# Performance work log

Hardware: AMD Instinct MI355X
Metric: run time of the kernel (lower is better)

## Reference

```python
import jax, jax.numpy as jnp
import numpy as np

N_NODES = 50000
N_EDGES = 800000
IN_DIM = 128
HID = 256
HEADS = 4
OUT_DIM = 128
NEG_SLOPE = 0.2


def gat_conv(x, src, dst, W, a_src, a_dst, b, heads, out_ch):
    """PyG-style GATConv: per-edge attention + segment softmax over dst."""
    N = x.shape[0]
    h = (x @ W).reshape(N, heads, out_ch)              # [N,H,C]
    alph_s = jnp.einsum('nhc,hc->nh', h, a_src)        # [N,H]
    alph_d = jnp.einsum('nhc,hc->nh', h, a_dst)        # [N,H]
    e = jax.nn.leaky_relu(alph_s[src] + alph_d[dst], NEG_SLOPE)  # [E,H]
    m = jax.lax.stop_gradient(jax.ops.segment_max(e, dst, num_segments=N))
    ex = jnp.exp(e - m[dst])
    s = jax.ops.segment_sum(ex, dst, num_segments=N)
    alpha = ex / (s[dst] + 1e-16)                      # [E,H]
    out = jax.ops.segment_sum(h[src] * alpha[:, :, None], dst, num_segments=N)
    return out.reshape(N, heads * out_ch) + b


def setup_inputs() -> dict:
    key = jax.random.key(0)
    ks = jax.random.split(key, 12)
    x = jax.random.normal(ks[0], (N_NODES, IN_DIM), dtype=jnp.float32)
    edge_index = jax.random.randint(ks[1], (2, N_EDGES), 0, N_NODES, dtype=jnp.int64)
    c1 = HID // HEADS  # 64
    sc1 = 1.0 / np.sqrt(IN_DIM)
    sc2 = 1.0 / np.sqrt(HID)
    W1 = jax.random.normal(ks[2], (IN_DIM, HID), dtype=jnp.float32) * sc1
    a1_src = jax.random.normal(ks[3], (HEADS, c1), dtype=jnp.float32) * sc1
    a1_dst = jax.random.normal(ks[4], (HEADS, c1), dtype=jnp.float32) * sc1
    b1 = jnp.zeros((HID,), dtype=jnp.float32)
    W2 = jax.random.normal(ks[5], (HID, OUT_DIM), dtype=jnp.float32) * sc2
    a2_src = jax.random.normal(ks[6], (1, OUT_DIM), dtype=jnp.float32) * sc2
    a2_dst = jax.random.normal(ks[7], (1, OUT_DIM), dtype=jnp.float32) * sc2
    b2 = jnp.zeros((OUT_DIM,), dtype=jnp.float32)
    return {"x": x, "edge_index": edge_index, "W1": W1, "a1_src": a1_src,
            "a1_dst": a1_dst, "b1": b1, "W2": W2, "a2_src": a2_src,
            "a2_dst": a2_dst, "b2": b2}


def reference(x, edge_index, W1, a1_src, a1_dst, b1, W2, a2_src, a2_dst, b2):
    N = x.shape[0]
    loops = jnp.arange(N, dtype=edge_index.dtype)
    # PyG default add_self_loops=True
    src = jnp.concatenate([edge_index[0], loops])
    dst = jnp.concatenate([edge_index[1], loops])
    h = jax.nn.relu(gat_conv(x, src, dst, W1, a1_src, a1_dst, b1, HEADS, HID // HEADS))
    # dropout is identity in eval mode
    return gat_conv(h, src, dst, W2, a2_src, a2_dst, b2, 1, OUT_DIM)
```

## Files before the change

### kernel.cpp

```cpp
#include <hip/hip_runtime.h>
#include <math.h>

#define NEG_SLOPE 0.2f
#define SLOTS 64
#define ECAP 63

typedef __attribute__((ext_vector_type(8))) short bf16x8;
typedef __attribute__((ext_vector_type(4))) float f32x4;
typedef __attribute__((ext_vector_type(2))) float f32x2;

__device__ __forceinline__ float lrelu(float t) {
    return t > 0.f ? t : NEG_SLOPE * t;
}
__device__ __forceinline__ unsigned short f2bf(float f) {
    unsigned u = __float_as_uint(f);
    unsigned r = (u + 0x7fff + ((u >> 16) & 1)) >> 16;
    return (unsigned short)r;
}
__device__ __forceinline__ f32x2 unpack2(unsigned v) {
    f32x2 r;
    r.x = __uint_as_float(v << 16);
    r.y = __uint_as_float(v & 0xffff0000u);
    return r;
}

__global__ void prep0(const float* __restrict__ W1, const float* __restrict__ a1s,
                      const float* __restrict__ a1d, float* __restrict__ vsd1,
                      const float* __restrict__ W2, const float* __restrict__ a2s,
                      const float* __restrict__ a2d, float* __restrict__ vsd2) {
    int i = blockIdx.x * 256 + threadIdx.x;
    if (i < 512) {
        int k = i >> 2, h = i & 3;
        float s = 0.f, d = 0.f;
        for (int c = 0; c < 64; c++) {
            float wv = W1[k * 256 + h * 64 + c];
            s += wv * a1s[h * 64 + c];
            d += wv * a1d[h * 64 + c];
        }
        vsd1[h * 128 + k] = s;
        vsd1[(4 + h) * 128 + k] = d;
    } else if (i < 768) {
        int j = i - 512;
        float s = 0.f, d = 0.f;
        for (int c = 0; c < 128; c++) {
            float wv = W2[j * 128 + c];
            s += wv * a2s[c];
            d += wv * a2d[c];
        }
        vsd2[j] = s;
        vsd2[256 + j] = d;
    }
}

__global__ void mega(const int* __restrict__ src, const int* __restrict__ dst,
                     int* __restrict__ cursor, unsigned short* __restrict__ eSrc,
                     const float* __restrict__ x, uint4* __restrict__ xb4,
                     const float* __restrict__ W1, unsigned short* __restrict__ W1t,
                     const float* __restrict__ W2, unsigned short* __restrict__ W2t,
                     const float* __restrict__ vsd1,
                     float* __restrict__ as1, float* __restrict__ ad1,
                     int E, int N, int bS, int bC, int bW1, int bW2) {
    __shared__ float vs[1024];
    const int b = blockIdx.x, t = threadIdx.x;
    if (b < bS) {
        int i4 = (b * 256 + t) * 4;
        if (i4 + 3 < E) {
            const int4 s4 = *(const int4*)(src + i4);
            const int4 d4 = *(const int4*)(dst + i4);
            int p0 = atomicAdd(&cursor[d4.x], 1);
            int p1 = atomicAdd(&cursor[d4.y], 1);
            int p2 = atomicAdd(&cursor[d4.z], 1);
            int p3 = atomicAdd(&cursor[d4.w], 1);
            if (p0 < ECAP) eSrc[(d4.x << 6) + p0] = (unsigned short)s4.x;
            if (p1 < ECAP) eSrc[(d4.y << 6) + p1] = (unsigned short)s4.y;
            if (p2 < ECAP) eSrc[(d4.z << 6) + p2] = (unsigned short)s4.z;
            if (p3 < ECAP) eSrc[(d4.w << 6) + p3] = (unsigned short)s4.w;
        } else {
            for (int k = i4; k < E && k < i4 + 4; k++) {
                int d = dst[k];
                int pos = atomicAdd(&cursor[d], 1);
                if (pos < ECAP) eSrc[(d << 6) + pos] = (unsigned short)src[k];
            }
        }
    } else if (b < bC) {
        int i = (b - bS) * 256 + t;
        if (i < N * 16) {
            const float4* x4 = (const float4*)x;
            float4 v0 = x4[2 * i], v1 = x4[2 * i + 1];
            uint4 o;
            o.x = (unsigned)f2bf(v0.x) | ((unsigned)f2bf(v0.y) << 16);
            o.y = (unsigned)f2bf(v0.z) | ((unsigned)f2bf(v0.w) << 16);
            o.z = (unsigned)f2bf(v1.x) | ((unsigned)f2bf(v1.y) << 16);
            o.w = (unsigned)f2bf(v1.z) | ((unsigned)f2bf(v1.w) << 16);
            xb4[i] = o;
        }
    } else if (b < bW1) {
        int i = (b - bC) * 256 + t;
        int n = i >> 7, k = i & 127;
        W1t[i] = f2bf(W1[k * 256 + n]);
    } else if (b < bW2) {
        int i = (b - bW1) * 256 + t;
        int n = i >> 8, k = i & 255;
        W2t[i] = f2bf(W2[k * 128 + n]);
    } else {
        for (int i = t; i < 1024; i += 256) vs[i] = vsd1[i];
        __syncthreads();
        int wave = t >> 6, lane = t & 63;
        int n = (b - bW2) * 4 + wave;
        if (n >= N) return;
        float acc[8];
#pragma unroll
        for (int j = 0; j < 8; j++) acc[j] = 0.f;
#pragma unroll
        for (int i = 0; i < 2; i++) {
            float xv = x[(size_t)n * 128 + i * 64 + lane];
#pragma unroll
            for (int j = 0; j < 8; j++) acc[j] += xv * vs[j * 128 + i * 64 + lane];
        }
#pragma unroll
        for (int off = 32; off > 0; off >>= 1) {
#pragma unroll
            for (int j = 0; j < 8; j++) acc[j] += __shfl_down(acc[j], off, 64);
        }
        if (lane == 0) {
#pragma unroll
            for (int h = 0; h < 4; h++) {
                as1[n * 4 + h] = acc[h];
                ad1[n * 4 + h] = acc[4 + h];
            }
        }
    }
}

template <int K, int N>
__global__ __launch_bounds__(256) void gemm_mfma(const unsigned short* __restrict__ A,
                                                 const unsigned short* __restrict__ Bt,
                                                 unsigned short* __restrict__ Cb, int M) {
    constexpr int LDT = 72;
    __shared__ __align__(16) short As[128 * LDT];
    __shared__ __align__(16) short Bs[64 * LDT];
    const int t = threadIdx.x;
    const int wave = t >> 6, lane = t & 63;
    const int row0 = blockIdx.x * 128;
    const int n0 = blockIdx.y * 64;

    f32x4 acc[2][4];
#pragma unroll
    for (int mt = 0; mt < 2; mt++)
#pragma unroll
        for (int nt = 0; nt < 4; nt++) acc[mt][nt] = (f32x4){0.f, 0.f, 0.f, 0.f};

    const int r = t >> 3, c8 = (t & 7) * 8;
    for (int kc = 0; kc < K; kc += 64) {
        const unsigned short* srcA = A + (size_t)row0 * K + kc;
#pragma unroll
        for (int p = 0; p < 4; p++) {
            int rr = r + p * 32;
            *(bf16x8*)&As[rr * LDT + c8] = *(const bf16x8*)&srcA[(size_t)rr * K + c8];
        }
        const unsigned short* srcB = Bt + (size_t)n0 * K + kc;
#pragma unroll
        for (int p = 0; p < 2; p++) {
            int rr = r + p * 32;
            *(bf16x8*)&Bs[rr * LDT + c8] = *(const bf16x8*)&srcB[(size_t)rr * K + c8];
        }
        __syncthreads();

        const int mbase = wave * 32 + (lane & 15);
        const int quad = lane >> 4;
#pragma unroll
        for (int ks = 0; ks < 2; ks++) {
            int ko = ks * 32 + quad * 8;
            bf16x8 a0 = *(const bf16x8*)&As[mbase * LDT + ko];
            bf16x8 a1 = *(const bf16x8*)&As[(mbase + 16) * LDT + ko];
#pragma unroll
            for (int nt = 0; nt < 4; nt++) {
                bf16x8 b = *(const bf16x8*)&Bs[((lane & 15) + nt * 16) * LDT + ko];
                acc[0][nt] = __builtin_amdgcn_mfma_f32_16x16x32_bf16(a0, b, acc[0][nt], 0, 0, 0);
                acc[1][nt] = __builtin_amdgcn_mfma_f32_16x16x32_bf16(a1, b, acc[1][nt], 0, 0, 0);
            }
        }
        __syncthreads();
    }

    const int colb = n0 + (lane & 15);
    const int rquad = (lane >> 4) * 4;
#pragma unroll
    for (int mt = 0; mt < 2; mt++) {
        int rb = row0 + wave * 32 + mt * 16 + rquad;
#pragma unroll
        for (int nt = 0; nt < 4; nt++) {
#pragma unroll
            for (int rr2 = 0; rr2 < 4; rr2++) {
                int row = rb + rr2;
                if (row < M) Cb[(size_t)row * N + colb + nt * 16] = f2bf(acc[mt][nt][rr2]);
            }
        }
    }
}

__global__ __launch_bounds__(256) void gemm1_head(
    const unsigned short* __restrict__ agg, const unsigned short* __restrict__ W1t,
    const float* __restrict__ b1, const float* __restrict__ vsd2,
    unsigned short* __restrict__ out1b, float* __restrict__ as2, float* __restrict__ ad2,
    int M, int Mpad) {
    constexpr int K = 128, LDT = 72;
    __shared__ __align__(16) short As[128 * LDT];
    __shared__ __align__(16) short Bs[64 * LDT];
    const int t = threadIdx.x;
    const int wave = t >> 6, lane = t & 63;
    const int row0 = blockIdx.x * 128;
    const int h = blockIdx.y;
    const unsigned short* A = agg + (size_t)h * Mpad * K;
    const unsigned short* Bt = W1t + (size_t)h * 64 * K;

    f32x4 acc[2][4];
#pragma unroll
    for (int mt = 0; mt < 2; mt++)
#pragma unroll
        for (int nt = 0; nt < 4; nt++) acc[mt][nt] = (f32x4){0.f, 0.f, 0.f, 0.f};

    const int r = t >> 3, c8 = (t & 7) * 8;
    for (int kc = 0; kc < K; kc += 64) {
        const unsigned short* srcA = A + (size_t)row0 * K + kc;
#pragma unroll
        for (int p = 0; p < 4; p++) {
            int rr = r + p * 32;
            *(bf16x8*)&As[rr * LDT + c8] = *(const bf16x8*)&srcA[(size_t)rr * K + c8];
        }
        const unsigned short* srcB = Bt + kc;
#pragma unroll
        for (int p = 0; p < 2; p++) {
            int rr = r + p * 32;
            *(bf16x8*)&Bs[rr * LDT + c8] = *(const bf16x8*)&srcB[(size_t)rr * K + c8];
        }
        __syncthreads();

        const int mbase = wave * 32 + (lane & 15);
        const int quad = lane >> 4;
#pragma unroll
        for (int ks = 0; ks < 2; ks++) {
            int ko = ks * 32 + quad * 8;
            bf16x8 a0 = *(const bf16x8*)&As[mbase * LDT + ko];
            bf16x8 a1 = *(const bf16x8*)&As[(mbase + 16) * LDT + ko];
#pragma unroll
            for (int nt = 0; nt < 4; nt++) {
                bf16x8 b = *(const bf16x8*)&Bs[((lane & 15) + nt * 16) * LDT + ko];
                acc[0][nt] = __builtin_amdgcn_mfma_f32_16x16x32_bf16(a0, b, acc[0][nt], 0, 0, 0);
                acc[1][nt] = __builtin_amdgcn_mfma_f32_16x16x32_bf16(a1, b, acc[1][nt], 0, 0, 0);
            }
        }
        __syncthreads();
    }

    const int col16 = lane & 15;
    const int grp = lane >> 4;
#pragma unroll
    for (int mt = 0; mt < 2; mt++) {
        int rb = row0 + wave * 32 + mt * 16 + grp * 4;
#pragma unroll
        for (int rr = 0; rr < 4; rr++) {
            int row = rb + rr;
            float ps = 0.f, pd = 0.f;
#pragma unroll
            for (int nt = 0; nt < 4; nt++) {
                int cg = h * 64 + col16 + nt * 16;
                float rres = acc[mt][nt][rr] + b1[cg];
                rres = fmaxf(rres, 0.f);
                if (row < M) out1b[(size_t)row * 256 + cg] = f2bf(rres);
                ps += rres * vsd2[cg];
                pd += rres * vsd2[256 + cg];
            }
#pragma unroll
            for (int mask = 1; mask < 16; mask <<= 1) {
                ps += __shfl_xor(ps, mask, 64);
                pd += __shfl_xor(pd, mask, 64);
            }
            if (col16 == 0 && row < M) {
                atomicAdd(&as2[row], ps);
                atomicAdd(&ad2[row], pd);
            }
        }
    }
}

__global__ __launch_bounds__(256) void fused_gather1(
    const int* __restrict__ cursor, const unsigned short* __restrict__ eSrc,
    const unsigned short* __restrict__ Xb,
    const float* __restrict__ as_, const float* __restrict__ ad_,
    unsigned short* __restrict__ agg, int N, int Mpad) {
    const int wv = threadIdx.x >> 6, lane = threadIdx.x & 63;
    const int half = lane >> 5, hl = lane & 31;
    const int d = blockIdx.x * 8 + wv * 2 + half;

    __shared__ float4 alS[4][2][64];
    __shared__ int offS[4][2][64];

    const bool vn = d < N;
    int deg = 0;
    if (vn) { deg = cursor[d]; if (deg > ECAP) deg = ECAP; }
    float4 adv = make_float4(0.f, 0.f, 0.f, 0.f);
    if (vn) adv = ((const float4*)ad_)[d];

    const int beg = d << 6;
    const int j0 = hl, j1 = hl + 32;
    const bool a0 = vn && (j0 <= deg), a1 = vn && (j1 <= deg);
    int s0 = vn ? d : 0, s1 = vn ? d : 0;
    if (vn && j0 < deg) s0 = eSrc[beg + j0];
    if (vn && j1 < deg) s1 = eSrc[beg + j1];
    float4 q0 = make_float4(0.f, 0.f, 0.f, 0.f), q1 = q0;
    if (a0) q0 = ((const float4*)as_)[s0];
    if (a1) q1 = ((const float4*)as_)[s1];

    float qa0[4] = {q0.x, q0.y, q0.z, q0.w};
    float qa1[4] = {q1.x, q1.y, q1.z, q1.w};
    float ad4[4] = {adv.x, adv.y, adv.z, adv.w};
    float e0[4], e1[4], m[4];
#pragma unroll
    for (int h = 0; h < 4; h++) {
        e0[h] = a0 ? lrelu(qa0[h] + ad4[h]) : -1e30f;
        e1[h] = a1 ? lrelu(qa1[h] + ad4[h]) : -1e30f;
        m[h] = fmaxf(e0[h], e1[h]);
    }
#pragma unroll
    for (int off = 1; off < 32; off <<= 1)
#pragma unroll
        for (int h = 0; h < 4; h++) m[h] = fmaxf(m[h], __shfl_xor(m[h], off, 64));
    float x0[4], x1[4], sum[4];
#pragma unroll
    for (int h = 0; h < 4; h++) {
        x0[h] = a0 ? __expf(e0[h] - m[h]) : 0.f;
        x1[h] = a1 ? __expf(e1[h] - m[h]) : 0.f;
        sum[h] = x0[h] + x1[h];
    }
#pragma unroll
    for (int off = 1; off < 32; off <<= 1)
#pragma unroll
        for (int h = 0; h < 4; h++) sum[h] += __shfl_xor(sum[h], off, 64);
    float ri[4];
#pragma unroll
    for (int h = 0; h < 4; h++) ri[h] = 1.f / (sum[h] + 1e-16f);

    alS[wv][half][j0] = make_float4(x0[0] * ri[0], x0[1] * ri[1], x0[2] * ri[2], x0[3] * ri[3]);
    alS[wv][half][j1] = make_float4(x1[0] * ri[0], x1[1] * ri[1], x1[2] * ri[2], x1[3] * ri[3]);
    offS[wv][half][j0] = s0 << 8;
    offS[wv][half][j1] = s1 << 8;

    int rows = vn ? deg + 1 : 0;
    { int o = __shfl_xor(rows, 32, 64); rows = rows > o ? rows : o; }

    const char* Xc = (const char*)Xb;
    const int myoff = hl * 8;
    f32x2 acc[4][2];
#pragma unroll
    for (int h = 0; h < 4; h++) { acc[h][0] = (f32x2){0.f, 0.f}; acc[h][1] = (f32x2){0.f, 0.f}; }

    int j = 0;
    for (; j + 3 < rows; j += 4) {
        int o0 = offS[wv][half][j], o1 = offS[wv][half][j + 1];
        int o2 = offS[wv][half][j + 2], o3 = offS[wv][half][j + 3];
        uint2 v0 = *(const uint2*)(Xc + o0 + myoff);
        uint2 v1 = *(const uint2*)(Xc + o1 + myoff);
        uint2 v2 = *(const uint2*)(Xc + o2 + myoff);
        uint2 v3 = *(const uint2*)(Xc + o3 + myoff);
        float4 al0 = alS[wv][half][j];
        float4 al1 = alS[wv][half][j + 1];
        float4 al2 = alS[wv][half][j + 2];
        float4 al3 = alS[wv][half][j + 3];
        {
            f32x2 lo = unpack2(v0.x), hi = unpack2(v0.y);
            acc[0][0] += al0.x * lo; acc[0][1] += al0.x * hi;
            acc[1][0] += al0.y * lo; acc[1][1] += al0.y * hi;
            acc[2][0] += al0.z * lo; acc[2][1] += al0.z * hi;
            acc[3][0] += al0.w * lo; acc[3][1] += al0.w * hi;
        }
        {
            f32x2 lo = unpack2(v1.x), hi = unpack2(v1.y);
            acc[0][0] += al1.x * lo; acc[0][1] += al1.x * hi;
            acc[1][0] += al1.y * lo; acc[1][1] += al1.y * hi;
            acc[2][0] += al1.z * lo; acc[2][1] += al1.z * hi;
            acc[3][0] += al1.w * lo; acc[3][1] += al1.w * hi;
        }
        {
            f32x2 lo = unpack2(v2.x), hi = unpack2(v2.y);
            acc[0][0] += al2.x * lo; acc[0][1] += al2.x * hi;
            acc[1][0] += al2.y * lo; acc[1][1] += al2.y * hi;
            acc[2][0] += al2.z * lo; acc[2][1] += al2.z * hi;
            acc[3][0] += al2.w * lo; acc[3][1] += al2.w * hi;
        }
        {
            f32x2 lo = unpack2(v3.x), hi = unpack2(v3.y);
            acc[0][0] += al3.x * lo; acc[0][1] += al3.x * hi;
            acc[1][0] += al3.y * lo; acc[1][1] += al3.y * hi;
            acc[2][0] += al3.z * lo; acc[2][1] += al3.z * hi;
            acc[3][0] += al3.w * lo; acc[3][1] += al3.w * hi;
        }
    }
    for (; j < rows; j++) {
        int o0 = offS[wv][half][j];
        uint2 v0 = *(const uint2*)(Xc + o0 + myoff);
        float4 al0 = alS[wv][half][j];
        f32x2 lo = unpack2(v0.x), hi = unpack2(v0.y);
        acc[0][0] += al0.x * lo; acc[0][1] += al0.x * hi;
        acc[1][0] += al0.y * lo; acc[1][1] += al0.y * hi;
        acc[2][0] += al0.z * lo; acc[2][1] += al0.z * hi;
        acc[3][0] += al0.w * lo; acc[3][1] += al0.w * hi;
    }

    if (vn) {
#pragma unroll
        for (int h = 0; h < 4; h++) {
            uint2 pack;
            pack.x = (unsigned)f2bf(acc[h][0].x) | ((unsigned)f2bf(acc[h][0].y) << 16);
            pack.y = (unsigned)f2bf(acc[h][1].x) | ((unsigned)f2bf(acc[h][1].y) << 16);
            ((uint2*)(agg + ((size_t)h * Mpad + d) * 128))[hl] = pack;
        }
    }
}

__global__ __launch_bounds__(256) void fused_gather2(
    const int* __restrict__ cursor, const unsigned short* __restrict__ eSrc,
    const unsigned short* __restrict__ Hb,
    const float* __restrict__ as_, const float* __restrict__ ad_,
    const float* __restrict__ b2, float* __restrict__ out, int N) {
    const int wv = threadIdx.x >> 6, lane = threadIdx.x & 63;
    const int half = lane >> 5, hl = lane & 31;
    const int d = blockIdx.x * 8 + wv * 2 + half;

    __shared__ float alS[4][2][64];
    __shared__ int offS[4][2][64];

    const bool vn = d < N;
    int deg = 0;
    if (vn) { deg = cursor[d]; if (deg > ECAP) deg = ECAP; }
    const float adv = vn ? ad_[d] : 0.f;

    const int beg = d << 6;
    const int j0 = hl, j1 = hl + 32;
    const bool a0 = vn && (j0 <= deg), a1 = vn && (j1 <= deg);
    int s0 = vn ? d : 0, s1 = vn ? d : 0;
    if (vn && j0 < deg) s0 = eSrc[beg + j0];
    if (vn && j1 < deg) s1 = eSrc[beg + j1];
    float e0 = a0 ? lrelu(as_[s0] + adv) : -1e30f;
    float e1 = a1 ? lrelu(as_[s1] + adv) : -1e30f;
    float m = fmaxf(e0, e1);
#pragma unroll
    for (int off = 1; off < 32; off <<= 1) m = fmaxf(m, __shfl_xor(m, off, 64));
    float x0 = a0 ? __expf(e0 - m) : 0.f;
    float x1 = a1 ? __expf(e1 - m) : 0.f;
    float sum = x0 + x1;
#pragma unroll
    for (int off = 1; off < 32; off <<= 1) sum += __shfl_xor(sum, off, 64);
    float ri = 1.f / (sum + 1e-16f);

    alS[wv][half][j0] = x0 * ri;
    alS[wv][half][j1] = x1 * ri;
    offS[wv][half][j0] = s0 << 8;
    offS[wv][half][j1] = s1 << 8;

    int rows = vn ? deg + 1 : 0;
    { int o = __shfl_xor(rows, 32, 64); rows = rows > o ? rows : o; }

    const char* Hc = (const char*)Hb;
    const int myoff = hl * 8;
    f32x2 acc0 = (f32x2){0.f, 0.f}, acc1 = (f32x2){0.f, 0.f};

    int j = 0;
    for (; j + 3 < rows; j += 4) {
        int o0 = offS[wv][half][j], o1 = offS[wv][half][j + 1];
        int o2 = offS[wv][half][j + 2], o3 = offS[wv][half][j + 3];
        uint2 v0 = *(const uint2*)(Hc + o0 + myoff);
        uint2 v1 = *(const uint2*)(Hc + o1 + myoff);
        uint2 v2 = *(const uint2*)(Hc + o2 + myoff);
        uint2 v3 = *(const uint2*)(Hc + o3 + myoff);
        float b0 = alS[wv][half][j], b1v = alS[wv][half][j + 1];
        float b2v = alS[wv][half][j + 2], b3 = alS[wv][half][j + 3];
        acc0 += b0 * unpack2(v0.x); acc1 += b0 * unpack2(v0.y);
        acc0 += b1v * unpack2(v1.x); acc1 += b1v * unpack2(v1.y);
        acc0 += b2v * unpack2(v2.x); acc1 += b2v * unpack2(v2.y);
        acc0 += b3 * unpack2(v3.x); acc1 += b3 * unpack2(v3.y);
    }
    for (; j < rows; j++) {
        int o0 = offS[wv][half][j];
        uint2 v0 = *(const uint2*)(Hc + o0 + myoff);
        float b0 = alS[wv][half][j];
        acc0 += b0 * unpack2(v0.x); acc1 += b0 * unpack2(v0.y);
    }

    if (vn) {
        float4 bb = ((const float4*)b2)[hl];
        float4 o;
        o.x = acc0.x + bb.x;
        o.y = acc0.y + bb.y;
        o.z = acc1.x + bb.z;
        o.w = acc1.y + bb.w;
        ((float4*)(out + (size_t)d * 128))[hl] = o;
    }
}

extern "C" void kernel_launch(void* const* d_in, const int* in_sizes, int n_in,
                              void* d_out, int out_size, void* d_ws, size_t ws_size,
                              hipStream_t stream) {
    const float* x   = (const float*)d_in[0];
    const int*   ei  = (const int*)d_in[1];
    const float* W1  = (const float*)d_in[2];
    const float* a1s = (const float*)d_in[3];
    const float* a1d = (const float*)d_in[4];
    const float* b1  = (const float*)d_in[5];
    const float* W2  = (const float*)d_in[6];
    const float* a2s = (const float*)d_in[7];
    const float* a2d = (const float*)d_in[8];
    const float* b2  = (const float*)d_in[9];

    const int N = in_sizes[0] / 128;
    const int E = in_sizes[1] / 2;
    const int* srcIdx = ei;
    const int* dstIdx = ei + E;
    float* out = (float*)d_out;

    const int MT = (N + 127) / 128;
    const int M_pad = MT * 128;

    char* w = (char*)d_ws;
    unsigned short* x_bf  = (unsigned short*)w; w += (size_t)N * 128 * 2;
    unsigned short* agg   = (unsigned short*)w; w += (size_t)4 * M_pad * 128 * 2;
    unsigned short* out1b = (unsigned short*)w; w += (size_t)M_pad * 256 * 2;
    unsigned short* h2b   = (unsigned short*)w; w += (size_t)N * 128 * 2;
    unsigned short* W1t   = (unsigned short*)w; w += (size_t)128 * 256 * 2;
    unsigned short* W2t   = (unsigned short*)w; w += (size_t)256 * 128 * 2;
    float* vsd1 = (float*)w; w += (size_t)128 * 8 * 4;
    float* vsd2 = (float*)w; w += (size_t)256 * 2 * 4;
    float* as1  = (float*)w; w += (size_t)N * 4 * 4;
    float* ad1  = (float*)w; w += (size_t)N * 4 * 4;
    float* as2  = (float*)w; w += (size_t)N * 4;
    float* ad2  = (float*)w; w += (size_t)N * 4;
    int* cursor = (int*)w;  w += (size_t)N * 4;
    unsigned short* eSrc = (unsigned short*)w; w += (size_t)N * SLOTS * 2;

    hipMemsetAsync(cursor, 0, (size_t)N * 4, stream);
    hipMemsetAsync(as2, 0, (size_t)N * 4, stream);
    hipMemsetAsync(ad2, 0, (size_t)N * 4, stream);

    prep0<<<3, 256, 0, stream>>>(W1, a1s, a1d, vsd1, W2, a2s, a2d, vsd2);

    {
        const int bS  = (E + 1023) / 1024;
        const int nC  = (N * 16 + 255) / 256;
        const int bC  = bS + nC;
        const int bW1 = bC + 128;
        const int bW2 = bW1 + 128;
        const int nG  = (N + 3) / 4;
        mega<<<bW2 + nG, 256, 0, stream>>>(srcIdx, dstIdx, cursor, eSrc,
                                           x, (uint4*)x_bf, W1, W1t, W2, W2t,
                                           vsd1, as1, ad1, E, N, bS, bC, bW1, bW2);
    }

    fused_gather1<<<(N + 7) / 8, 256, 0, stream>>>(cursor, eSrc, x_bf, as1, ad1, agg, N, M_pad);
    gemm1_head<<<dim3(MT, 4), 256, 0, stream>>>(agg, W1t, b1, vsd2, out1b, as2, ad2, N, M_pad);

    gemm_mfma<256, 128><<<dim3(MT, 2), 256, 0, stream>>>(out1b, W2t, h2b, N);
    fused_gather2<<<(N + 7) / 8, 256, 0, stream>>>(cursor, eSrc, h2b, as2, ad2, b2, out, N);
}
```

Before: 294.1 us.

## Build CSR via two-pass bucketed binning with LDS atomics

Replaces per-edge global atomics on the per-node cursor with a two-level scheme. Each block counts edges per 128-node bucket in shared memory, reserves ranges with one global atomic per bucket, and scatters packed (local dst, src) words into bucket bins. A new build_csr kernel then places edges into per-node slots in LDS and writes them out coalesced. This targets scattered global atomic contention and uncoalesced 2-byte writes, at the cost of an extra kernel launch, bin traffic through the reused agg buffer, and a fixed per-bucket capacity that could drop edges on skewed graphs.

```diff
diff --git a/kernel.cpp b/kernel.cpp
--- a/kernel.cpp
+++ b/kernel.cpp
@@ -4,6 +4,8 @@
 #define NEG_SLOPE 0.2f
 #define SLOTS 64
 #define ECAP 63
+#define NBMAX 391
+#define BCAP 2432
 
 typedef __attribute__((ext_vector_type(8))) short bf16x8;
 typedef __attribute__((ext_vector_type(4))) float f32x4;
@@ -52,38 +54,72 @@
     }
 }
 
+#define EMIT(dd, ss)                                                     \
+    {                                                                    \
+        int bk_ = (dd) >> 7;                                             \
+        int pos_ = atomicAdd(&cntS[bk_], 1);                             \
+        if (pos_ < BCAP)                                                 \
+            bin[(size_t)bk_ * BCAP + pos_] =                             \
+                ((unsigned)((dd) & 127) << 16) | (unsigned)(ss);         \
+    }
+
 __global__ void mega(const int* __restrict__ src, const int* __restrict__ dst,
-                     int* __restrict__ cursor, unsigned short* __restrict__ eSrc,
+                     int* __restrict__ gcur, unsigned* __restrict__ bin,
                      const float* __restrict__ x, uint4* __restrict__ xb4,
                      const float* __restrict__ W1, unsigned short* __restrict__ W1t,
                      const float* __restrict__ W2, unsigned short* __restrict__ W2t,
                      const float* __restrict__ vsd1,
                      float* __restrict__ as1, float* __restrict__ ad1,
-                     int E, int N, int bS, int bC, int bW1, int bW2) {
+                     int E, int N, int nb, int bP1, int bC, int bW1, int bW2) {
     __shared__ float vs[1024];
+    __shared__ int cntS[NBMAX];
     const int b = blockIdx.x, t = threadIdx.x;
-    if (b < bS) {
-        int i4 = (b * 256 + t) * 4;
-        if (i4 + 3 < E) {
-            const int4 s4 = *(const int4*)(src + i4);
-            const int4 d4 = *(const int4*)(dst + i4);
-            int p0 = atomicAdd(&cursor[d4.x], 1);
-            int p1 = atomicAdd(&cursor[d4.y], 1);
-            int p2 = atomicAdd(&cursor[d4.z], 1);
-            int p3 = atomicAdd(&cursor[d4.w], 1);
-            if (p0 < ECAP) eSrc[(d4.x << 6) + p0] = (unsigned short)s4.x;
-            if (p1 < ECAP) eSrc[(d4.y << 6) + p1] = (unsigned short)s4.y;
-            if (p2 < ECAP) eSrc[(d4.z << 6) + p2] = (unsigned short)s4.z;
-            if (p3 < ECAP) eSrc[(d4.w << 6) + p3] = (unsigned short)s4.w;
-        } else {
-            for (int k = i4; k < E && k < i4 + 4; k++) {
-                int d = dst[k];
-                int pos = atomicAdd(&cursor[d], 1);
-                if (pos < ECAP) eSrc[(d << 6) + pos] = (unsigned short)src[k];
-            }
-        }
+    if (b < bP1) {
+        for (int i = t; i < nb; i += 256) cntS[i] = 0;
+        __syncthreads();
+        const int4* s4p = (const int4*)src;
+        const int4* d4p = (const int4*)dst;
+        const int E4 = E >> 2;
+        int4 sv[4], dv[4];
+        bool act[4];
+#pragma unroll
+        for (int i = 0; i < 4; i++) {
+            int idx = b * 1024 + i * 256 + t;
+            act[i] = idx < E4;
+            sv[i] = act[i] ? s4p[idx] : (int4){0, 0, 0, 0};
+            dv[i] = act[i] ? d4p[idx] : (int4){0, 0, 0, 0};
+        }
+        int exd = -1, exs = 0;
+        if (b == 0 && (E4 << 2) + t < E) {
+            exd = dst[(E4 << 2) + t];
+            exs = src[(E4 << 2) + t];
+        }
+#pragma unroll
+        for (int i = 0; i < 4; i++)
+            if (act[i]) {
+                atomicAdd(&cntS[dv[i].x >> 7], 1);
+                atomicAdd(&cntS[dv[i].y >> 7], 1);
+                atomicAdd(&cntS[dv[i].z >> 7], 1);
+                atomicAdd(&cntS[dv[i].w >> 7], 1);
+            }
+        if (exd >= 0) atomicAdd(&cntS[exd >> 7], 1);
+        __syncthreads();
+        for (int i = t; i < nb; i += 256) {
+            int c = cntS[i];
+            cntS[i] = c ? atomicAdd(&gcur[i], c) : 0;
+        }
+        __syncthreads();
+#pragma unroll
+        for (int i = 0; i < 4; i++)
+            if (act[i]) {
+                EMIT(dv[i].x, sv[i].x);
+                EMIT(dv[i].y, sv[i].y);
+                EMIT(dv[i].z, sv[i].z);
+                EMIT(dv[i].w, sv[i].w);
+            }
+        if (exd >= 0) EMIT(exd, exs);
     } else if (b < bC) {
-        int i = (b - bS) * 256 + t;
+        int i = (b - bP1) * 256 + t;
         if (i < N * 16) {
             const float4* x4 = (const float4*)x;
             float4 v0 = x4[2 * i], v1 = x4[2 * i + 1];
@@ -130,6 +166,32 @@
             }
         }
     }
+}
+
+__global__ __launch_bounds__(256) void build_csr(const int* __restrict__ gcur,
+                                                 const unsigned* __restrict__ bin,
+                                                 unsigned short* __restrict__ eSrc,
+                                                 int* __restrict__ cursor) {
+    __shared__ unsigned short slotS[128 * 64];
+    __shared__ int lc[128];
+    const int b = blockIdx.x, t = threadIdx.x;
+    if (t < 128) lc[t] = 0;
+    __syncthreads();
+    int cnt = gcur[b];
+    if (cnt > BCAP) cnt = BCAP;
+    const unsigned* bb = bin + (size_t)b * BCAP;
+    for (int i = t; i < cnt; i += 256) {
+        unsigned e = bb[i];
+        int dl = e >> 16;
+        int p = atomicAdd(&lc[dl], 1);
+        if (p < ECAP) slotS[(dl << 6) + p] = (unsigned short)(e & 0xffff);
+    }
+    __syncthreads();
+    const uint4* sp = (const uint4*)slotS;
+    uint4* dp = (uint4*)(eSrc + ((size_t)b << 13));
+#pragma unroll
+    for (int i = 0; i < 4; i++) dp[t + i * 256] = sp[t + i * 256];
+    if (t < 128) cursor[(b << 7) + t] = lc[t];
 }
 
 template <int K, int N>
@@ -520,6 +582,7 @@
 
     const int MT = (N + 127) / 128;
     const int M_pad = MT * 128;
+    const int nb = (N + 127) >> 7;
 
     char* w = (char*)d_ws;
     unsigned short* x_bf  = (unsigned short*)w; w += (size_t)N * 128 * 2;
@@ -534,26 +597,30 @@
     float* ad1  = (float*)w; w += (size_t)N * 4 * 4;
     float* as2  = (float*)w; w += (size_t)N * 4;
     float* ad2  = (float*)w; w += (size_t)N * 4;
-    int* cursor = (int*)w;  w += (size_t)N * 4;
-    unsigned short* eSrc = (unsigned short*)w; w += (size_t)N * SLOTS * 2;
-
-    hipMemsetAsync(cursor, 0, (size_t)N * 4, stream);
+    int* cursor = (int*)w;  w += (size_t)M_pad * 4;
+    unsigned short* eSrc = (unsigned short*)w; w += (size_t)M_pad * SLOTS * 2;
+    int* gcur = (int*)w; w += (size_t)nb * 4;
+    unsigned* bin = (unsigned*)agg;
+
+    hipMemsetAsync(gcur, 0, (size_t)nb * 4, stream);
     hipMemsetAsync(as2, 0, (size_t)N * 4, stream);
     hipMemsetAsync(ad2, 0, (size_t)N * 4, stream);
 
     prep0<<<3, 256, 0, stream>>>(W1, a1s, a1d, vsd1, W2, a2s, a2d, vsd2);
 
     {
-        const int bS  = (E + 1023) / 1024;
+        const int bP1 = (E / 4 + 1023) / 1024;
         const int nC  = (N * 16 + 255) / 256;
-        const int bC  = bS + nC;
+        const int bC  = bP1 + nC;
         const int bW1 = bC + 128;
         const int bW2 = bW1 + 128;
         const int nG  = (N + 3) / 4;
-        mega<<<bW2 + nG, 256, 0, stream>>>(srcIdx, dstIdx, cursor, eSrc,
+        mega<<<bW2 + nG, 256, 0, stream>>>(srcIdx, dstIdx, gcur, bin,
                                            x, (uint4*)x_bf, W1, W1t, W2, W2t,
-                                           vsd1, as1, ad1, E, N, bS, bC, bW1, bW2);
-    }
+                                           vsd1, as1, ad1, E, N, nb, bP1, bC, bW1, bW2);
+    }
+
+    build_csr<<<nb, 256, 0, stream>>>(gcur, bin, eSrc, cursor);
 
     fused_gather1<<<(N + 7) / 8, 256, 0, stream>>>(cursor, eSrc, x_bf, as1, ad1, agg, N, M_pad);
     gemm1_head<<<dim3(MT, 4), 256, 0, stream>>>(agg, W1t, b1, vsd2, out1b, as2, ad2, N, M_pad);
```

New measurement: 249.1 us. -15.3%, faster.
